# Kernel optimization log

Measured on AMD Instinct MI355X. Metric: run time of the kernel, lower is better.

## Reference

```python
import jax, jax.numpy as jnp
import numpy as np

L = 3        # num_hidden_layers
H = 512      # hidden_features
DIN = 4      # in_features
D = DIN - 1  # u-branch input dim
N = 65536    # batch of query points


def setup_inputs() -> dict:
    key = jax.random.key(0)
    ks = jax.random.split(key, 16)

    def w(k, shape, fan_in):
        # kaiming-normal-ish init (relu), matches init_weights_normal in spirit
        return jax.random.normal(k, shape, jnp.float32) * (2.0 / fan_in) ** 0.5

    return {
        "coords": jax.random.normal(ks[0], (N, DIN), jnp.float32),
        # net_u: (D->H), then (H->H) x (L-1)
        "Wu0": w(ks[1], (D, H), D), "bu0": jnp.zeros((H,), jnp.float32),
        "Wu": w(ks[2], (L - 1, H, H), H), "bu": jnp.zeros((L - 1, H), jnp.float32),
        # net_zu_u: (H->H) x L
        "Wzuu": w(ks[3], (L, H, H), H), "bzuu": jnp.zeros((L, H), jnp.float32),
        # net_z_zu: (H->H) x (L-1), last (H->1), no bias
        "Wzzu": w(ks[4], (L - 1, H, H), H), "Wzzu_last": w(ks[5], (H, 1), H),
        # net_yu_u: (D->1), then (H->1) x L
        "Wyuu0": w(ks[6], (D, 1), D), "byuu0": jnp.zeros((1,), jnp.float32),
        "Wyuu": w(ks[7], (L, H, 1), H), "byuu": jnp.zeros((L, 1), jnp.float32),
        # net_z_yu: (1->H) x L, last (1->1), no bias
        "Wzyu": w(ks[8], (L, 1, H), 1), "Wzyu_last": w(ks[9], (1, 1), 1),
        # net_z_u: (D->H), (H->H) x (L-1), last (H->1)
        "Wzu0": w(ks[10], (D, H), D), "bzu0": jnp.zeros((H,), jnp.float32),
        "Wzu": w(ks[11], (L - 1, H, H), H), "bzu": jnp.zeros((L - 1, H), jnp.float32),
        "Wzu_last": w(ks[12], (H, 1), H), "bzu_last": jnp.zeros((1,), jnp.float32),
        # learned scalar scales
        "p": jnp.float32(0.1), "pu": jnp.float32(0.1), "pzu": jnp.float32(0.1),
    }


def reference(coords, Wu0, bu0, Wu, bu, Wzuu, bzuu, Wzzu, Wzzu_last,
              Wyuu0, byuu0, Wyuu, byuu, Wzyu, Wzyu_last,
              Wzu0, bzu0, Wzu, bzu, Wzu_last, bzu_last, p, pu, pzu):
    relu = jax.nn.relu  # nonlinearity='relu' -> nl == nl_u == relu; dropout inactive (eval)
    y = coords[..., -1:]   # [N, 1]
    u = coords[..., :-1]   # [N, D]
    # layer 0
    z = (u @ Wzu0 + bzu0) + (y * (u @ Wyuu0 + byuu0)) @ Wzyu[0]  # [N, H]
    z = relu(10.0 * p * z)
    u = relu(10.0 * pu * (u @ Wu0 + bu0))  # [N, H]
    for i in range(1, L + 1):
        zz = z * relu(10.0 * pzu * (u @ Wzuu[i - 1] + bzuu[i - 1]))
        t1 = zz @ (Wzzu[i - 1] if i < L else Wzzu_last)
        t2 = (u @ Wzu[i - 1] + bzu[i - 1]) if i < L else (u @ Wzu_last + bzu_last)
        yy = y * (u @ Wyuu[i - 1] + byuu[i - 1])  # [N, 1]
        t3 = yy @ (Wzyu[i] if i < L else Wzyu_last)
        z = t1 + t2 + t3
        if i == L:
            return z  # [N, 1]
        z_out = relu(10.0 * p * z)
        u = relu(10.0 * pu * (u @ Wu[i - 1] + bu[i - 1]))
        z = z_out
    return z
```

## Files before the change

### kernel.cpp

```cpp
#include <hip/hip_runtime.h>
#include <stdint.h>
#include <stddef.h>


typedef float  f32x4 __attribute__((ext_vector_type(4)));
typedef __bf16 bf16x8 __attribute__((ext_vector_type(8)));

__device__ __forceinline__ int act_idx(int row, int k){
  return ((k>>5)<<11) | ((row>>4)<<9) | (((k>>3)&3)<<7) | ((row&15)<<3) | (k&7);
}

__global__ void prep_weights(const float* __restrict__ Wzuu, const float* __restrict__ Wzzu,
                             const float* __restrict__ Wzu,  const float* __restrict__ Wu,
                             __bf16* __restrict__ Wb)
{
  int gid = blockIdx.x * 256 + threadIdx.x;
  int m   = gid >> 16;
  int rem = gid & 65535;
  int k   = rem >> 7;
  int j0  = (rem & 127) << 2;
  const float* src;
  if      (m < 3) src = Wzuu + (size_t)m     * 262144;
  else if (m < 5) src = Wzzu + (size_t)(m-3) * 262144;
  else if (m < 7) src = Wzu  + (size_t)(m-5) * 262144;
  else            src = Wu   + (size_t)(m-7) * 262144;
  const float4 v = *(const float4*)(src + k*512 + j0);
  const int base = m << 18;
  #pragma unroll
  for (int e = 0; e < 4; ++e){
    const int j = j0 + e;
    const float x = (e==0) ? v.x : (e==1) ? v.y : (e==2) ? v.z : v.w;
    const int off = ((k>>5)<<14) | ((j>>4)<<9)
                  | ((((j&15) | (((k>>3)&3)<<4)))<<3) | (k&7);
    Wb[base + off] = (__bf16)x;
  }
}

__device__ __forceinline__ void gemm_acc(const __bf16* __restrict__ a_lds,
                                         const __bf16* __restrict__ wb,
                                         f32x4 acc[4][4],
                                         int wv, int lane)
{
  const __bf16* wp = wb + ((wv<<2)<<9) + (lane<<3);
  bf16x8 b[4][4];
  bf16x8 a[2][4];
  #pragma unroll
  for (int d = 0; d < 4; ++d)
    #pragma unroll
    for (int jt = 0; jt < 4; ++jt)
      b[d][jt] = __builtin_nontemporal_load((const bf16x8*)(wp + (d<<14) + (jt<<9)));
  #pragma unroll
  for (int rt = 0; rt < 4; ++rt)
    a[0][rt] = *(const bf16x8*)(a_lds + (rt<<9) + (lane<<3));
  #pragma unroll
  for (int kt = 0; kt < 16; ++kt){
    if (kt < 15){
      #pragma unroll
      for (int rt = 0; rt < 4; ++rt)
        a[(kt+1)&1][rt] = *(const bf16x8*)(a_lds + ((kt+1)<<11) + (rt<<9) + (lane<<3));
    }
    #pragma unroll
    for (int jt = 0; jt < 4; ++jt)
      #pragma unroll
      for (int rt = 0; rt < 4; ++rt)
        acc[rt][jt] = __builtin_amdgcn_mfma_f32_16x16x32_bf16(a[kt&1][rt], b[kt&3][jt], acc[rt][jt], 0, 0, 0);
    if (kt + 4 < 16){
      #pragma unroll
      for (int jt = 0; jt < 4; ++jt)
        b[kt&3][jt] = __builtin_nontemporal_load((const bf16x8*)(wp + ((kt+4)<<14) + (jt<<9)));
    }
  }
}

__global__ __launch_bounds__(512, 2) void fc_fused(
    const float* __restrict__ coords,
    const __bf16* __restrict__ Wb,
    const float* __restrict__ Wu0,  const float* __restrict__ bu0,
    const float* __restrict__ bu,
    const float* __restrict__ bzuu,
    const float* __restrict__ Wzzu_last,
    const float* __restrict__ Wyuu0, const float* __restrict__ byuu0,
    const float* __restrict__ Wyuu,  const float* __restrict__ byuu,
    const float* __restrict__ Wzyu,  const float* __restrict__ Wzyu_last,
    const float* __restrict__ Wzu0,  const float* __restrict__ bzu0,
    const float* __restrict__ bzu,
    const float* __restrict__ Wzu_last, const float* __restrict__ bzu_last,
    const float* __restrict__ p, const float* __restrict__ pu, const float* __restrict__ pzu,
    float* __restrict__ out)
{
  __shared__ __align__(16) __bf16 u_lds [32768];
  __shared__ __align__(16) __bf16 zz_lds[32768];
  __shared__ float sp_lds[2][64];

  const int tid  = threadIdx.x;
  const int lane = tid & 63;
  const int wv   = tid >> 6;
  const int n0   = blockIdx.x << 6;

  const float P  = 10.f * p[0];
  const float PU = 10.f * pu[0];
  const float PZ = 10.f * pzu[0];

  const float y_l = coords[(size_t)(n0 + lane)*4 + 3];

  for (int s = tid; s < 4096; s += 512){
    const int row = s >> 6;
    const int k0  = (s & 63) << 3;
    const float* c = coords + (size_t)(n0 + row)*4;
    const float c0 = c[0], c1 = c[1], c2 = c[2], yy = c[3];
    const float s0 = c0*Wyuu0[0] + c1*Wyuu0[1] + c2*Wyuu0[2] + byuu0[0];
    bf16x8 pu8, pz8;
    #pragma unroll
    for (int e = 0; e < 8; ++e){
      const int k = k0 + e;
      const float uv = c0*Wu0[k]  + c1*Wu0[512+k]  + c2*Wu0[1024+k]  + bu0[k];
      pu8[e] = (__bf16)fmaxf(PU*uv, 0.f);
      const float zv = c0*Wzu0[k] + c1*Wzu0[512+k] + c2*Wzu0[1024+k] + bzu0[k]
                     + yy*s0*Wzyu[k];
      pz8[e] = (__bf16)fmaxf(P*zv, 0.f);
    }
    *(bf16x8*)(u_lds  + act_idx(row, k0)) = pu8;
    *(bf16x8*)(zz_lds + act_idx(row, k0)) = pz8;
  }
  __syncthreads();

  f32x4 acc[4][4];

  for (int it = 0; it < 3; ++it){
    const __bf16* w_p1 = Wb + ((size_t)it     << 18);
    const __bf16* w_zz = Wb + ((size_t)(3+it) << 18);
    const __bf16* w_zu = Wb + ((size_t)(5+it) << 18);
    const __bf16* w_u  = Wb + ((size_t)(7+it) << 18);

    {
      const float* wc = Wyuu + (it<<9);
      const int rt = wv & 3;
      const int kh = wv >> 2;
      float pp = 0.f;
      #pragma unroll
      for (int t = 0; t < 8; ++t){
        const int kt = (kh<<3) + t;
        const int k0 = (kt<<5) + ((lane>>4)<<3);
        bf16x8 v = *(const bf16x8*)(u_lds + (kt<<11) + (rt<<9) + (lane<<3));
        const float4 w0 = *(const float4*)(wc + k0);
        const float4 w1 = *(const float4*)(wc + k0 + 4);
        pp += (float)v[0]*w0.x + (float)v[1]*w0.y + (float)v[2]*w0.z + (float)v[3]*w0.w
            + (float)v[4]*w1.x + (float)v[5]*w1.y + (float)v[6]*w1.z + (float)v[7]*w1.w;
      }
      pp += __shfl_xor(pp, 16);
      pp += __shfl_xor(pp, 32);
      if (lane < 16) sp_lds[kh][(rt<<4) + lane] = pp;
    }

    #pragma unroll
    for (int rt = 0; rt < 4; ++rt)
      #pragma unroll
      for (int jt = 0; jt < 4; ++jt)
        acc[rt][jt] = (f32x4){0.f,0.f,0.f,0.f};
    gemm_acc(u_lds, w_p1, acc, wv, lane);
    #pragma unroll
    for (int jt = 0; jt < 4; ++jt){
      const int col = (wv<<6) + (jt<<4) + (lane & 15);
      const float bz = bzuu[(it<<9) + col];
      #pragma unroll
      for (int rt = 0; rt < 4; ++rt){
        #pragma unroll
        for (int rr = 0; rr < 4; ++rr){
          const int row = (rt<<4) + ((lane>>4)<<2) + rr;
          const int idx = act_idx(row, col);
          const float zold = (float)zz_lds[idx];
          const float t    = acc[rt][jt][rr] + bz;
          zz_lds[idx] = (__bf16)(zold * fmaxf(PZ*t, 0.f));
        }
      }
    }
    __syncthreads();

    if (it < 2){
      #pragma unroll
      for (int rt = 0; rt < 4; ++rt)
        #pragma unroll
        for (int jt = 0; jt < 4; ++jt)
          acc[rt][jt] = (f32x4){0.f,0.f,0.f,0.f};
      gemm_acc(zz_lds, w_zz, acc, wv, lane);
      gemm_acc(u_lds,  w_zu, acc, wv, lane);
      __syncthreads();

      const float by_it = byuu[it];
      float ysr[4][4];
      #pragma unroll
      for (int rt = 0; rt < 4; ++rt)
        #pragma unroll
        for (int rr = 0; rr < 4; ++rr){
          const int row = (rt<<4) + ((lane>>4)<<2) + rr;
          ysr[rt][rr] = __shfl(y_l, row) * (sp_lds[0][row] + sp_lds[1][row] + by_it);
        }
      #pragma unroll
      for (int jt = 0; jt < 4; ++jt){
        const int col = (wv<<6) + (jt<<4) + (lane & 15);
        const float bz  = bzu[(it<<9) + col];
        const float wzy = Wzyu[((it+1)<<9) + col];
        #pragma unroll
        for (int rt = 0; rt < 4; ++rt){
          #pragma unroll
          for (int rr = 0; rr < 4; ++rr){
            const int row = (rt<<4) + ((lane>>4)<<2) + rr;
            const float zn = acc[rt][jt][rr] + bz + ysr[rt][rr]*wzy;
            zz_lds[act_idx(row, col)] = (__bf16)fmaxf(P*zn, 0.f);
          }
        }
      }

      #pragma unroll
      for (int rt = 0; rt < 4; ++rt)
        #pragma unroll
        for (int jt = 0; jt < 4; ++jt)
          acc[rt][jt] = (f32x4){0.f,0.f,0.f,0.f};
      gemm_acc(u_lds, w_u, acc, wv, lane);
      __syncthreads();
      #pragma unroll
      for (int jt = 0; jt < 4; ++jt){
        const int col = (wv<<6) + (jt<<4) + (lane & 15);
        const float bb = bu[(it<<9) + col];
        #pragma unroll
        for (int rt = 0; rt < 4; ++rt){
          #pragma unroll
          for (int rr = 0; rr < 4; ++rr){
            const int row = (rt<<4) + ((lane>>4)<<2) + rr;
            u_lds[act_idx(row, col)] = (__bf16)fmaxf(PU*(acc[rt][jt][rr] + bb), 0.f);
          }
        }
      }
      __syncthreads();
    } else {
      const int row = tid >> 3;
      const int q   = tid & 7;
      float av = 0.f, au = 0.f;
      for (int kb = q*8; kb < q*8 + 8; ++kb){
        const int k0 = kb << 3;
        bf16x8 vz = *(const bf16x8*)(zz_lds + act_idx(row, k0));
        bf16x8 vu = *(const bf16x8*)(u_lds  + act_idx(row, k0));
        #pragma unroll
        for (int e = 0; e < 8; ++e){
          av += (float)vz[e] * Wzzu_last[k0+e];
          au += (float)vu[e] * Wzu_last [k0+e];
        }
      }
      float tot = av + au;
      tot += __shfl_xor(tot, 1);
      tot += __shfl_xor(tot, 2);
      tot += __shfl_xor(tot, 4);
      const float sv = sp_lds[0][row] + sp_lds[1][row] + byuu[2];
      const float yv = __shfl(y_l, row & 63);
      if (q == 0)
        out[n0 + row] = tot + bzu_last[0] + yv*sv*Wzyu_last[0];
    }
  }
}

extern "C" void kernel_launch(void* const* d_in, const int* in_sizes, int n_in,
                              void* d_out, int out_size, void* d_ws, size_t ws_size,
                              hipStream_t stream)
{
  const float* coords    = (const float*)d_in[0];
  const float* Wu0       = (const float*)d_in[1];
  const float* bu0       = (const float*)d_in[2];
  const float* Wu        = (const float*)d_in[3];
  const float* bu        = (const float*)d_in[4];
  const float* Wzuu      = (const float*)d_in[5];
  const float* bzuu      = (const float*)d_in[6];
  const float* Wzzu      = (const float*)d_in[7];
  const float* Wzzu_last = (const float*)d_in[8];
  const float* Wyuu0     = (const float*)d_in[9];
  const float* byuu0     = (const float*)d_in[10];
  const float* Wyuu      = (const float*)d_in[11];
  const float* byuu      = (const float*)d_in[12];
  const float* Wzyu      = (const float*)d_in[13];
  const float* Wzyu_last = (const float*)d_in[14];
  const float* Wzu0      = (const float*)d_in[15];
  const float* bzu0      = (const float*)d_in[16];
  const float* Wzu       = (const float*)d_in[17];
  const float* bzu       = (const float*)d_in[18];
  const float* Wzu_last  = (const float*)d_in[19];
  const float* bzu_last  = (const float*)d_in[20];
  const float* p         = (const float*)d_in[21];
  const float* pu        = (const float*)d_in[22];
  const float* pzu       = (const float*)d_in[23];

  __bf16* Wb = (__bf16*)d_ws;

  prep_weights<<<2304, 256, 0, stream>>>(Wzuu, Wzzu, Wzu, Wu, Wb);

  fc_fused<<<1024, 512, 0, stream>>>(
      coords, Wb,
      Wu0, bu0, bu, bzuu, Wzzu_last,
      Wyuu0, byuu0, Wyuu, byuu, Wzyu, Wzyu_last,
      Wzu0, bzu0, bzu, Wzu_last, bzu_last,
      p, pu, pzu,
      (float*)d_out);
}
```

Measured before the change: 389.3 us.

## Stage weight tiles through LDS with async global_load_lds and barrier pipelining

Replaces each wave's private register streaming of weight tiles with a block-shared LDS staging ring. global_load_lds direct-to-LDS copies are pipelined three stages ahead and gated by vmcnt waits and per-step barriers, and MFMA blocks run at raised priority. The weight layout is re-permuted so that each 8 KB chunk matches one staging slot. The ysr/sv precomputation moves earlier so its scratch can reuse the stage buffer. The goal is less redundant global/L2 traffic and lower register pressure, at the cost of a barrier on every quarter-k step.

New measurement: 593.7 us. 1.52x slower.

```diff
diff --git a/kernel.cpp b/kernel.cpp
--- a/kernel.cpp
+++ b/kernel.cpp
@@ -5,6 +5,14 @@
 
 typedef float  f32x4 __attribute__((ext_vector_type(4)));
 typedef __bf16 bf16x8 __attribute__((ext_vector_type(8)));
+
+#define S_BARRIER()  __builtin_amdgcn_s_barrier()
+#define SCHED_PIN()  __builtin_amdgcn_sched_barrier(0)
+#define VMCNT2()     asm volatile("s_waitcnt vmcnt(2)" ::: "memory")
+#define VMCNT0()     asm volatile("s_waitcnt vmcnt(0)" ::: "memory")
+#define GLDS16(g,l)  __builtin_amdgcn_global_load_lds( \
+    (const __attribute__((address_space(1))) void*)(g), \
+    (__attribute__((address_space(3))) void*)(l), 16, 0, 0)
 
 __device__ __forceinline__ int act_idx(int row, int k){
   return ((k>>5)<<11) | ((row>>4)<<9) | (((k>>3)&3)<<7) | ((row&15)<<3) | (k&7);
@@ -30,44 +38,47 @@
   for (int e = 0; e < 4; ++e){
     const int j = j0 + e;
     const float x = (e==0) ? v.x : (e==1) ? v.y : (e==2) ? v.z : v.w;
-    const int off = ((k>>5)<<14) | ((j>>4)<<9)
+    const int off = ((k>>5)<<14) | (((j>>4)&3)<<12) | ((j>>6)<<9)
                   | ((((j&15) | (((k>>3)&3)<<4)))<<3) | (k&7);
     Wb[base + off] = (__bf16)x;
   }
 }
 
-__device__ __forceinline__ void gemm_acc(const __bf16* __restrict__ a_lds,
-                                         const __bf16* __restrict__ wb,
-                                         f32x4 acc[4][4],
-                                         int wv, int lane)
+__device__ __forceinline__ void gemm_staged(const __bf16* __restrict__ a_lds,
+                                            const __bf16* __restrict__ wb,
+                                            __bf16* stage,
+                                            f32x4 acc[4][4],
+                                            int wv, int lane, int tid)
 {
-  const __bf16* wp = wb + ((wv<<2)<<9) + (lane<<3);
-  bf16x8 b[4][4];
-  bf16x8 a[2][4];
+  const char* gsrc = (const char*)wb + tid*16;
+  char*       ldst = (char*)stage + tid*16;
   #pragma unroll
-  for (int d = 0; d < 4; ++d)
+  for (int i = 0; i < 3; ++i)
+    GLDS16(gsrc + i*8192, ldst + i*8192);
+
+  #pragma unroll 1
+  for (int kt = 0; kt < 16; ++kt){
+    bf16x8 afr[4];
     #pragma unroll
-    for (int jt = 0; jt < 4; ++jt)
-      b[d][jt] = __builtin_nontemporal_load((const bf16x8*)(wp + (d<<14) + (jt<<9)));
-  #pragma unroll
-  for (int rt = 0; rt < 4; ++rt)
-    a[0][rt] = *(const bf16x8*)(a_lds + (rt<<9) + (lane<<3));
-  #pragma unroll
-  for (int kt = 0; kt < 16; ++kt){
-    if (kt < 15){
+    for (int q = 0; q < 4; ++q){
+      if (q == 3 && kt == 15) { VMCNT0(); } else { VMCNT2(); }
+      S_BARRIER();
+      SCHED_PIN();
+      if (q == 0){
+        #pragma unroll
+        for (int rt = 0; rt < 4; ++rt)
+          afr[rt] = *(const bf16x8*)(a_lds + (kt<<11) + (rt<<9) + (lane<<3));
+      }
+      bf16x8 bfr = *(const bf16x8*)(stage + (q<<12) + (wv<<9) + (lane<<3));
+      if (q == 0 || kt < 15){
+        const int tgt = (kt<<2) + q + 3;
+        GLDS16(gsrc + tgt*8192, ldst + ((tgt&3)<<13));
+      }
+      __builtin_amdgcn_s_setprio(1);
       #pragma unroll
       for (int rt = 0; rt < 4; ++rt)
-        a[(kt+1)&1][rt] = *(const bf16x8*)(a_lds + ((kt+1)<<11) + (rt<<9) + (lane<<3));
-    }
-    #pragma unroll
-    for (int jt = 0; jt < 4; ++jt)
-      #pragma unroll
-      for (int rt = 0; rt < 4; ++rt)
-        acc[rt][jt] = __builtin_amdgcn_mfma_f32_16x16x32_bf16(a[kt&1][rt], b[kt&3][jt], acc[rt][jt], 0, 0, 0);
-    if (kt + 4 < 16){
-      #pragma unroll
-      for (int jt = 0; jt < 4; ++jt)
-        b[kt&3][jt] = __builtin_nontemporal_load((const bf16x8*)(wp + ((kt+4)<<14) + (jt<<9)));
+        acc[rt][q] = __builtin_amdgcn_mfma_f32_16x16x32_bf16(afr[rt], bfr, acc[rt][q], 0, 0, 0);
+      __builtin_amdgcn_s_setprio(0);
     }
   }
 }
@@ -90,7 +101,7 @@
 {
   __shared__ __align__(16) __bf16 u_lds [32768];
   __shared__ __align__(16) __bf16 zz_lds[32768];
-  __shared__ float sp_lds[2][64];
+  __shared__ __align__(16) __bf16 stage [16384];
 
   const int tid  = threadIdx.x;
   const int lane = tid & 63;
@@ -132,6 +143,7 @@
     const __bf16* w_zu = Wb + ((size_t)(5+it) << 18);
     const __bf16* w_u  = Wb + ((size_t)(7+it) << 18);
 
+    float* sp = (float*)stage;
     {
       const float* wc = Wyuu + (it<<9);
       const int rt = wv & 3;
@@ -149,15 +161,36 @@
       }
       pp += __shfl_xor(pp, 16);
       pp += __shfl_xor(pp, 32);
-      if (lane < 16) sp_lds[kh][(rt<<4) + lane] = pp;
-    }
+      if (lane < 16) sp[(kh<<6) + (rt<<4) + lane] = pp;
+    }
+    __syncthreads();
+
+    float ysr[4][4];
+    float sv_f = 0.f, yv_f = 0.f;
+    {
+      const float by_it = byuu[it];
+      if (it < 2){
+        #pragma unroll
+        for (int rt = 0; rt < 4; ++rt)
+          #pragma unroll
+          for (int rr = 0; rr < 4; ++rr){
+            const int row = (rt<<4) + ((lane>>4)<<2) + rr;
+            ysr[rt][rr] = __shfl(y_l, row) * (sp[row] + sp[64+row] + by_it);
+          }
+      } else {
+        const int row = tid >> 3;
+        sv_f = sp[row] + sp[64+row] + by_it;
+        yv_f = __shfl(y_l, row & 63);
+      }
+    }
+    __syncthreads();
 
     #pragma unroll
     for (int rt = 0; rt < 4; ++rt)
       #pragma unroll
       for (int jt = 0; jt < 4; ++jt)
         acc[rt][jt] = (f32x4){0.f,0.f,0.f,0.f};
-    gemm_acc(u_lds, w_p1, acc, wv, lane);
+    gemm_staged(u_lds, w_p1, stage, acc, wv, lane, tid);
     #pragma unroll
     for (int jt = 0; jt < 4; ++jt){
       const int col = (wv<<6) + (jt<<4) + (lane & 15);
@@ -182,19 +215,10 @@
         #pragma unroll
         for (int jt = 0; jt < 4; ++jt)
           acc[rt][jt] = (f32x4){0.f,0.f,0.f,0.f};
-      gemm_acc(zz_lds, w_zz, acc, wv, lane);
-      gemm_acc(u_lds,  w_zu, acc, wv, lane);
+      gemm_staged(zz_lds, w_zz, stage, acc, wv, lane, tid);
+      gemm_staged(u_lds,  w_zu, stage, acc, wv, lane, tid);
       __syncthreads();
 
-      const float by_it = byuu[it];
-      float ysr[4][4];
-      #pragma unroll
-      for (int rt = 0; rt < 4; ++rt)
-        #pragma unroll
-        for (int rr = 0; rr < 4; ++rr){
-          const int row = (rt<<4) + ((lane>>4)<<2) + rr;
-          ysr[rt][rr] = __shfl(y_l, row) * (sp_lds[0][row] + sp_lds[1][row] + by_it);
-        }
       #pragma unroll
       for (int jt = 0; jt < 4; ++jt){
         const int col = (wv<<6) + (jt<<4) + (lane & 15);
@@ -216,7 +240,7 @@
         #pragma unroll
         for (int jt = 0; jt < 4; ++jt)
           acc[rt][jt] = (f32x4){0.f,0.f,0.f,0.f};
-      gemm_acc(u_lds, w_u, acc, wv, lane);
+      gemm_staged(u_lds, w_u, stage, acc, wv, lane, tid);
       __syncthreads();
       #pragma unroll
       for (int jt = 0; jt < 4; ++jt){
@@ -250,10 +274,8 @@
       tot += __shfl_xor(tot, 1);
       tot += __shfl_xor(tot, 2);
       tot += __shfl_xor(tot, 4);
-      const float sv = sp_lds[0][row] + sp_lds[1][row] + byuu[2];
-      const float yv = __shfl(y_l, row & 63);
       if (q == 0)
-        out[n0 + row] = tot + bzu_last[0] + yv*sv*Wzyu_last[0];
+        out[n0 + row] = tot + bzu_last[0] + yv_f*sv_f*Wzyu_last[0];
     }
   }
 }
```
